# Performance work log

Measured on AMD Instinct MI355X. Metric: run time of the kernel, lower is better.

Reference implementation:

```python
import jax, jax.numpy as jnp
import numpy as np

GRID_SIZE = 5
SPLINE_ORDER = 3
GRID_RANGE = (-1.0, 1.0)
EPS = 1e-8


def _make_grid():
    h = (GRID_RANGE[1] - GRID_RANGE[0]) / GRID_SIZE
    # knots: [-spline_order, ..., grid_size + spline_order] * h + lo  -> 12 values
    return jnp.arange(-SPLINE_ORDER, GRID_SIZE + SPLINE_ORDER + 1, dtype=jnp.float32) * h + GRID_RANGE[0]


def _bspline_basis(x, grid):
    # x: [N, in]  ->  bases: [N, in, num_basis] with num_basis = grid_size + spline_order
    xe = x[..., None]                                   # [N, in, 1]
    bases = ((xe >= grid[:-1]) & (xe < grid[1:])).astype(x.dtype)  # [N, in, 11]
    for k in range(1, SPLINE_ORDER + 1):
        left = (xe - grid[: -(k + 1)]) / (grid[k:-1] - grid[: -(k + 1)] + EPS) * bases[..., :-1]
        right = (grid[k + 1:] - xe) / (grid[k + 1:] - grid[1:-k] + EPS) * bases[..., 1:]
        bases = left + right
    return bases                                        # [N, in, 8]


def setup_inputs() -> dict:
    key = jax.random.key(0)
    k1, k2, k3 = jax.random.split(key, 3)
    in_f, out_f, num_basis = 1024, 1024, GRID_SIZE + SPLINE_ORDER
    N = 4096
    x = jax.random.normal(k1, (N, in_f), dtype=jnp.float32)
    base_weight = jax.random.normal(k2, (out_f, in_f), dtype=jnp.float32) * (1.0 / np.sqrt(in_f))
    base_bias = jnp.zeros((out_f,), dtype=jnp.float32)
    spline_weight = jax.random.normal(k3, (out_f, in_f, num_basis), dtype=jnp.float32) * (1.0 / np.sqrt(in_f))
    return {"x": x, "base_weight": base_weight, "base_bias": base_bias, "spline_weight": spline_weight}


def reference(x, base_weight, base_bias, spline_weight):
    grid = _make_grid()
    # base path: SiLU(x) @ W_base^T + b
    base_out = jax.nn.silu(x) @ base_weight.T + base_bias          # [N, out]
    # spline path: Cox-de Boor basis then contraction over (in, basis)
    basis = _bspline_basis(x, grid)                                 # [N, in, 8]
    spline_out = jnp.einsum('nib,oib->no', basis, spline_weight)    # [N, out]
    return base_out + spline_out
```

## Files before the change

### kernel.cpp

```cpp
#include <hip/hip_runtime.h>
#include <hip/hip_bf16.h>
#include <stdint.h>

#define IN_F 1024
#define OUT_F 1024
#define NB 8
#define KDIM (IN_F + IN_F * NB)
#define NROWS 4096
#define SLICE_ELEMS (NROWS * OUT_F)
#define PREP_BLOCKS ((NROWS * IN_F) / 256)
#define WCONV_BLOCKS ((OUT_F * KDIM) / (4 * 256))

typedef __attribute__((ext_vector_type(8))) short bf16x8;
typedef __attribute__((ext_vector_type(4))) short bf16x4;
typedef __attribute__((ext_vector_type(4))) float f32x4;

__device__ __forceinline__ void bspline8(float x, float b8[8]) {
  float u = (x + 2.2f) * 2.5f;
  bool in = (u >= 0.0f) && (u < 11.0f);
  float uc = fminf(fmaxf(u, 0.0f), 10.99f);
  int i = (int)uc;
  float f = uc - (float)i;
  float g = 1.0f - f;
  float f2 = f * f, f3 = f2 * f;
  const float s = 1.0f / 6.0f;
  float v0 = f3 * s;
  float v1 = (-3.0f * f3 + 3.0f * f2 + 3.0f * f + 1.0f) * s;
  float v2 = (3.0f * f3 - 6.0f * f2 + 4.0f) * s;
  float v3 = g * g * g * s;
#pragma unroll
  for (int j = 0; j < 8; ++j) {
    int d = i - j;
    float r = (d == 0) ? v0 : (d == 1) ? v1 : (d == 2) ? v2 : (d == 3) ? v3 : 0.0f;
    b8[j] = in ? r : 0.0f;
  }
}

__global__ void prep_all_kernel(const float* __restrict__ x, const float* __restrict__ bw,
                                const float* __restrict__ sw, __hip_bfloat16* __restrict__ A,
                                __hip_bfloat16* __restrict__ W) {
  if (blockIdx.x < PREP_BLOCKS) {
    int idx = blockIdx.x * 256 + threadIdx.x;
    int n = idx >> 10;
    int i = idx & 1023;
    float xv = x[idx];
    float sl = xv / (1.0f + __expf(-xv));
    __hip_bfloat16* row = A + (size_t)n * KDIM;
    row[i] = __float2bfloat16(sl);
    float b8[8];
    bspline8(xv, b8);
    alignas(16) __hip_bfloat16 tmp[8];
#pragma unroll
    for (int c = 0; c < 8; ++c) tmp[c] = __float2bfloat16(b8[c]);
    *(bf16x8*)(row + IN_F + i * 8) = *(const bf16x8*)tmp;
  } else {
    int v = (blockIdx.x - PREP_BLOCKS) * 256 + threadIdx.x;
    int e = v * 4;
    int o = e / KDIM;
    int k = e - o * KDIM;
    float4 val = (k < IN_F) ? *(const float4*)(bw + o * IN_F + k)
                            : *(const float4*)(sw + (size_t)o * (IN_F * NB) + (k - IN_F));
    alignas(8) __hip_bfloat16 t[4];
    t[0] = __float2bfloat16(val.x);
    t[1] = __float2bfloat16(val.y);
    t[2] = __float2bfloat16(val.z);
    t[3] = __float2bfloat16(val.w);
    *(bf16x4*)(W + e) = *(const bf16x4*)t;
  }
}

__global__ __launch_bounds__(256) void gemm_kernel(const __hip_bfloat16* __restrict__ A,
                                                   const __hip_bfloat16* __restrict__ W,
                                                   float* __restrict__ dst,
                                                   const float* __restrict__ bias,
                                                   int kslice, int use_bias) {
  __shared__ __hip_bfloat16 lA[2][128 * 64];
  __shared__ __hip_bfloat16 lB[2][128 * 64];
  const int tid = threadIdx.x;
  const int wave = tid >> 6;
  const int lane = tid & 63;
  const int bm = blockIdx.x * 128;
  const int bn = blockIdx.y * 128;
  const int z = blockIdx.z;
  float* __restrict__ d = dst + (size_t)z * SLICE_ELEMS;
  const int kbeg = z * kslice;
  const int iters = kslice / 64;
  const int srow = lane & 15;
  const int skc = (lane >> 4) * 8;
  const int wm = (wave & 1) * 64;
  const int wn = (wave >> 1) * 64;
  const int r = lane & 15;
  const int quad = lane >> 4;

  const int g0 = wave * 2;
  const __hip_bfloat16* gA[2];
  const __hip_bfloat16* gB[2];
  gA[0] = A + (size_t)(bm + g0 * 16 + srow) * KDIM + kbeg + skc;
  gA[1] = gA[0] + (size_t)16 * KDIM;
  gB[0] = W + (size_t)(bn + g0 * 16 + srow) * KDIM + kbeg + skc;
  gB[1] = gB[0] + (size_t)16 * KDIM;

  f32x4 acc[4][4];
#pragma unroll
  for (int a = 0; a < 4; ++a)
#pragma unroll
    for (int b = 0; b < 4; ++b) acc[a][b] = (f32x4){0.f, 0.f, 0.f, 0.f};

#define STAGE(IT, BUF)                                                                             \
  do {                                                                                             \
    const int koff = (IT) * 64;                                                                    \
    _Pragma("unroll") for (int h = 0; h < 2; ++h) {                                                \
      _Pragma("unroll") for (int s = 0; s < 2; ++s) {                                              \
        const __hip_bfloat16* srcA = gA[h] + koff + s * 32;                                        \
        const __hip_bfloat16* srcB = gB[h] + koff + s * 32;                                        \
        __hip_bfloat16* dA = &lA[BUF][((g0 + h) * 2 + s) * 512];                                   \
        __hip_bfloat16* dB = &lB[BUF][((g0 + h) * 2 + s) * 512];                                   \
        __builtin_amdgcn_global_load_lds((const __attribute__((address_space(1))) void*)srcA,      \
                                         (__attribute__((address_space(3))) void*)dA, 16, 0, 0);   \
        __builtin_amdgcn_global_load_lds((const __attribute__((address_space(1))) void*)srcB,      \
                                         (__attribute__((address_space(3))) void*)dB, 16, 0, 0);   \
      }                                                                                            \
    }                                                                                              \
  } while (0)

  STAGE(0, 0);
  __syncthreads();

  for (int it = 0; it < iters; ++it) {
    const int p = it & 1;
    if (it + 1 < iters) STAGE(it + 1, p ^ 1);

#pragma unroll
    for (int s = 0; s < 2; ++s) {
      bf16x8 af[4], bfr[4];
#pragma unroll
      for (int t = 0; t < 4; ++t) {
        af[t] = *(const bf16x8*)&lA[p][(((wm >> 4) + t) * 2 + s) * 512 + lane * 8];
        bfr[t] = *(const bf16x8*)&lB[p][(((wn >> 4) + t) * 2 + s) * 512 + lane * 8];
      }
#pragma unroll
      for (int tm = 0; tm < 4; ++tm)
#pragma unroll
        for (int tn = 0; tn < 4; ++tn)
          acc[tm][tn] =
              __builtin_amdgcn_mfma_f32_16x16x32_bf16(af[tm], bfr[tn], acc[tm][tn], 0, 0, 0);
    }

    __syncthreads();
  }
#undef STAGE

#pragma unroll
  for (int tm = 0; tm < 4; ++tm) {
#pragma unroll
    for (int tn = 0; tn < 4; ++tn) {
      const int col = bn + wn + tn * 16 + r;
      const float bv = use_bias ? bias[col] : 0.0f;
#pragma unroll
      for (int reg = 0; reg < 4; ++reg) {
        const int rowi = bm + wm + tm * 16 + quad * 4 + reg;
        d[(size_t)rowi * OUT_F + col] = acc[tm][tn][reg] + bv;
      }
    }
  }
}

__global__ void reduce_kernel(const float* __restrict__ P, const float* __restrict__ bias,
                              float* __restrict__ out, int S) {
  int v = blockIdx.x * 256 + threadIdx.x;
  int e = v * 4;
  int o = e & (OUT_F - 1);
  float4 acc = *(const float4*)(bias + o);
  for (int s = 0; s < S; ++s) {
    float4 p = *(const float4*)(P + (size_t)s * SLICE_ELEMS + e);
    acc.x += p.x;
    acc.y += p.y;
    acc.z += p.z;
    acc.w += p.w;
  }
  *(float4*)(out + e) = acc;
}

__global__ void kan_fallback(const float* __restrict__ x, const float* __restrict__ bw,
                             const float* __restrict__ bb, const float* __restrict__ sw,
                             float* __restrict__ out) {
  __shared__ float act[KDIM];
  int n = blockIdx.x;
  for (int i = threadIdx.x; i < IN_F; i += 256) {
    float xv = x[(size_t)n * IN_F + i];
    act[i] = xv / (1.0f + __expf(-xv));
    float b8[8];
    bspline8(xv, b8);
#pragma unroll
    for (int c = 0; c < 8; ++c) act[IN_F + i * 8 + c] = b8[c];
  }
  __syncthreads();
  for (int o = threadIdx.x; o < OUT_F; o += 256) {
    float s = bb[o];
    const float* wbp = bw + (size_t)o * IN_F;
    for (int k = 0; k < IN_F; ++k) s += act[k] * wbp[k];
    const float* wsp = sw + (size_t)o * (IN_F * NB);
    for (int k = 0; k < IN_F * NB; ++k) s += act[IN_F + k] * wsp[k];
    out[(size_t)n * OUT_F + o] = s;
  }
}

extern "C" void kernel_launch(void* const* d_in, const int* in_sizes, int n_in, void* d_out,
                              int out_size, void* d_ws, size_t ws_size, hipStream_t stream) {
  const float* x = (const float*)d_in[0];
  const float* bw = (const float*)d_in[1];
  const float* bb = (const float*)d_in[2];
  const float* sw = (const float*)d_in[3];
  float* out = (float*)d_out;

  const size_t needA = (size_t)NROWS * KDIM * 2;
  const size_t needW = (size_t)OUT_F * KDIM * 2;
  const size_t sliceB = (size_t)SLICE_ELEMS * 4;
  if (ws_size < needA + needW) {
    kan_fallback<<<NROWS, 256, 0, stream>>>(x, bw, bb, sw, out);
    return;
  }
  __hip_bfloat16* A = (__hip_bfloat16*)d_ws;
  __hip_bfloat16* W = (__hip_bfloat16*)((char*)d_ws + needA);
  float* P = (float*)((char*)d_ws + needA + needW);
  const size_t avail = ws_size - needA - needW;
  int S = (avail >= 2 * sliceB) ? 2 : 1;

  prep_all_kernel<<<PREP_BLOCKS + WCONV_BLOCKS, 256, 0, stream>>>(x, bw, sw, A, W);
  if (S == 1) {
    gemm_kernel<<<dim3(NROWS / 128, OUT_F / 128, 1), 256, 0, stream>>>(A, W, out, bb, KDIM, 1);
  } else {
    gemm_kernel<<<dim3(NROWS / 128, OUT_F / 128, S), 256, 0, stream>>>(A, W, P, bb, KDIM / S, 0);
    reduce_kernel<<<SLICE_ELEMS / (4 * 256), 256, 0, stream>>>(P, bb, out, S);
  }
}
```

Before: 258.6 us.

## Use 256x256 tiles with split-K of four and atomic accumulation into output

The GEMM block tile grows from 128x128 to 256x256 with 512 threads, and each wave computes an 8x4 grid of 16x16 MFMA tiles. K is split four ways and partial results are added straight into the output with float atomics. The output is pre-initialised with the bias inside the prep kernel, so the partial-slice buffer and the separate reduce kernel go away. The larger tile raises arithmetic intensity per LDS byte but uses 128KB of LDS per block and more registers, which may limit occupancy. The atomics add contention and make the summation order non-deterministic.

```diff
diff --git a/kernel.cpp b/kernel.cpp
--- a/kernel.cpp
+++ b/kernel.cpp
@@ -8,8 +8,11 @@
 #define KDIM (IN_F + IN_F * NB)
 #define NROWS 4096
 #define SLICE_ELEMS (NROWS * OUT_F)
+#define INIT_BLOCKS (SLICE_ELEMS / (4 * 256))
 #define PREP_BLOCKS ((NROWS * IN_F) / 256)
 #define WCONV_BLOCKS ((OUT_F * KDIM) / (4 * 256))
+#define SPLIT 4
+#define KSLICE (KDIM / SPLIT)
 
 typedef __attribute__((ext_vector_type(8))) short bf16x8;
 typedef __attribute__((ext_vector_type(4))) short bf16x4;
@@ -37,10 +40,16 @@
 }
 
 __global__ void prep_all_kernel(const float* __restrict__ x, const float* __restrict__ bw,
-                                const float* __restrict__ sw, __hip_bfloat16* __restrict__ A,
-                                __hip_bfloat16* __restrict__ W) {
-  if (blockIdx.x < PREP_BLOCKS) {
-    int idx = blockIdx.x * 256 + threadIdx.x;
+                                const float* __restrict__ sw, const float* __restrict__ bb,
+                                __hip_bfloat16* __restrict__ A, __hip_bfloat16* __restrict__ W,
+                                float* __restrict__ out) {
+  if (blockIdx.x < INIT_BLOCKS) {
+    int v = blockIdx.x * 256 + threadIdx.x;
+    int e = v * 4;
+    int o = e & (OUT_F - 1);
+    *(float4*)(out + e) = *(const float4*)(bb + o);
+  } else if (blockIdx.x < INIT_BLOCKS + PREP_BLOCKS) {
+    int idx = (blockIdx.x - INIT_BLOCKS) * 256 + threadIdx.x;
     int n = idx >> 10;
     int i = idx & 1023;
     float xv = x[idx];
@@ -54,7 +63,7 @@
     for (int c = 0; c < 8; ++c) tmp[c] = __float2bfloat16(b8[c]);
     *(bf16x8*)(row + IN_F + i * 8) = *(const bf16x8*)tmp;
   } else {
-    int v = (blockIdx.x - PREP_BLOCKS) * 256 + threadIdx.x;
+    int v = (blockIdx.x - INIT_BLOCKS - PREP_BLOCKS) * 256 + threadIdx.x;
     int e = v * 4;
     int o = e / KDIM;
     int k = e - o * KDIM;
@@ -69,58 +78,53 @@
   }
 }
 
-__global__ __launch_bounds__(256) void gemm_kernel(const __hip_bfloat16* __restrict__ A,
-                                                   const __hip_bfloat16* __restrict__ W,
-                                                   float* __restrict__ dst,
-                                                   const float* __restrict__ bias,
-                                                   int kslice, int use_bias) {
-  __shared__ __hip_bfloat16 lA[2][128 * 64];
-  __shared__ __hip_bfloat16 lB[2][128 * 64];
+__global__ __launch_bounds__(512, 2) void gemm_kernel(const __hip_bfloat16* __restrict__ A,
+                                                      const __hip_bfloat16* __restrict__ W,
+                                                      float* __restrict__ out) {
+  __shared__ __hip_bfloat16 lA[2][256 * 64];
+  __shared__ __hip_bfloat16 lB[2][256 * 64];
   const int tid = threadIdx.x;
   const int wave = tid >> 6;
   const int lane = tid & 63;
-  const int bm = blockIdx.x * 128;
-  const int bn = blockIdx.y * 128;
-  const int z = blockIdx.z;
-  float* __restrict__ d = dst + (size_t)z * SLICE_ELEMS;
-  const int kbeg = z * kslice;
-  const int iters = kslice / 64;
+  const int bm = blockIdx.x * 256;
+  const int bn = blockIdx.y * 256;
+  const int kbeg = blockIdx.z * KSLICE;
+  const int iters = KSLICE / 64;
   const int srow = lane & 15;
   const int skc = (lane >> 4) * 8;
-  const int wm = (wave & 1) * 64;
-  const int wn = (wave >> 1) * 64;
+  const int wmi = wave & 1;
+  const int wni = wave >> 1;
   const int r = lane & 15;
   const int quad = lane >> 4;
 
-  const int g0 = wave * 2;
   const __hip_bfloat16* gA[2];
   const __hip_bfloat16* gB[2];
-  gA[0] = A + (size_t)(bm + g0 * 16 + srow) * KDIM + kbeg + skc;
+  gA[0] = A + (size_t)(bm + wave * 32 + srow) * KDIM + kbeg + skc;
   gA[1] = gA[0] + (size_t)16 * KDIM;
-  gB[0] = W + (size_t)(bn + g0 * 16 + srow) * KDIM + kbeg + skc;
+  gB[0] = W + (size_t)(bn + wave * 32 + srow) * KDIM + kbeg + skc;
   gB[1] = gB[0] + (size_t)16 * KDIM;
 
-  f32x4 acc[4][4];
-#pragma unroll
-  for (int a = 0; a < 4; ++a)
+  f32x4 acc[8][4];
+#pragma unroll
+  for (int a = 0; a < 8; ++a)
 #pragma unroll
     for (int b = 0; b < 4; ++b) acc[a][b] = (f32x4){0.f, 0.f, 0.f, 0.f};
 
-#define STAGE(IT, BUF)                                                                             \
-  do {                                                                                             \
-    const int koff = (IT) * 64;                                                                    \
-    _Pragma("unroll") for (int h = 0; h < 2; ++h) {                                                \
-      _Pragma("unroll") for (int s = 0; s < 2; ++s) {                                              \
-        const __hip_bfloat16* srcA = gA[h] + koff + s * 32;                                        \
-        const __hip_bfloat16* srcB = gB[h] + koff + s * 32;                                        \
-        __hip_bfloat16* dA = &lA[BUF][((g0 + h) * 2 + s) * 512];                                   \
-        __hip_bfloat16* dB = &lB[BUF][((g0 + h) * 2 + s) * 512];                                   \
-        __builtin_amdgcn_global_load_lds((const __attribute__((address_space(1))) void*)srcA,      \
-                                         (__attribute__((address_space(3))) void*)dA, 16, 0, 0);   \
-        __builtin_amdgcn_global_load_lds((const __attribute__((address_space(1))) void*)srcB,      \
-                                         (__attribute__((address_space(3))) void*)dB, 16, 0, 0);   \
-      }                                                                                            \
-    }                                                                                              \
+#define STAGE(IT, BUF)                                                                           \
+  do {                                                                                           \
+    const int koff = (IT) * 64;                                                                  \
+    _Pragma("unroll") for (int h = 0; h < 2; ++h) {                                              \
+      _Pragma("unroll") for (int s = 0; s < 2; ++s) {                                            \
+        const __hip_bfloat16* srcA = gA[h] + koff + s * 32;                                      \
+        const __hip_bfloat16* srcB = gB[h] + koff + s * 32;                                      \
+        __hip_bfloat16* dA = &lA[BUF][((wave * 2 + h) * 2 + s) * 512];                           \
+        __hip_bfloat16* dB = &lB[BUF][((wave * 2 + h) * 2 + s) * 512];                           \
+        __builtin_amdgcn_global_load_lds((const __attribute__((address_space(1))) void*)srcA,    \
+                                         (__attribute__((address_space(3))) void*)dA, 16, 0, 0); \
+        __builtin_amdgcn_global_load_lds((const __attribute__((address_space(1))) void*)srcB,    \
+                                         (__attribute__((address_space(3))) void*)dB, 16, 0, 0); \
+      }                                                                                          \
+    }                                                                                            \
   } while (0)
 
   STAGE(0, 0);
@@ -132,14 +136,15 @@
 
 #pragma unroll
     for (int s = 0; s < 2; ++s) {
-      bf16x8 af[4], bfr[4];
-#pragma unroll
-      for (int t = 0; t < 4; ++t) {
-        af[t] = *(const bf16x8*)&lA[p][(((wm >> 4) + t) * 2 + s) * 512 + lane * 8];
-        bfr[t] = *(const bf16x8*)&lB[p][(((wn >> 4) + t) * 2 + s) * 512 + lane * 8];
-      }
-#pragma unroll
-      for (int tm = 0; tm < 4; ++tm)
+      bf16x8 af[8], bfr[4];
+#pragma unroll
+      for (int t = 0; t < 8; ++t)
+        af[t] = *(const bf16x8*)&lA[p][(((wmi * 8 + t) * 2 + s)) * 512 + lane * 8];
+#pragma unroll
+      for (int t = 0; t < 4; ++t)
+        bfr[t] = *(const bf16x8*)&lB[p][(((wni * 4 + t) * 2 + s)) * 512 + lane * 8];
+#pragma unroll
+      for (int tm = 0; tm < 8; ++tm)
 #pragma unroll
         for (int tn = 0; tn < 4; ++tn)
           acc[tm][tn] =
@@ -151,34 +156,17 @@
 #undef STAGE
 
 #pragma unroll
-  for (int tm = 0; tm < 4; ++tm) {
+  for (int tm = 0; tm < 8; ++tm) {
 #pragma unroll
     for (int tn = 0; tn < 4; ++tn) {
-      const int col = bn + wn + tn * 16 + r;
-      const float bv = use_bias ? bias[col] : 0.0f;
+      const int col = bn + wni * 64 + tn * 16 + r;
 #pragma unroll
       for (int reg = 0; reg < 4; ++reg) {
-        const int rowi = bm + wm + tm * 16 + quad * 4 + reg;
-        d[(size_t)rowi * OUT_F + col] = acc[tm][tn][reg] + bv;
+        const int rowi = bm + wmi * 128 + tm * 16 + quad * 4 + reg;
+        atomicAdd(out + (size_t)rowi * OUT_F + col, acc[tm][tn][reg]);
       }
     }
   }
-}
-
-__global__ void reduce_kernel(const float* __restrict__ P, const float* __restrict__ bias,
-                              float* __restrict__ out, int S) {
-  int v = blockIdx.x * 256 + threadIdx.x;
-  int e = v * 4;
-  int o = e & (OUT_F - 1);
-  float4 acc = *(const float4*)(bias + o);
-  for (int s = 0; s < S; ++s) {
-    float4 p = *(const float4*)(P + (size_t)s * SLICE_ELEMS + e);
-    acc.x += p.x;
-    acc.y += p.y;
-    acc.z += p.z;
-    acc.w += p.w;
-  }
-  *(float4*)(out + e) = acc;
 }
 
 __global__ void kan_fallback(const float* __restrict__ x, const float* __restrict__ bw,
@@ -215,22 +203,14 @@
 
   const size_t needA = (size_t)NROWS * KDIM * 2;
   const size_t needW = (size_t)OUT_F * KDIM * 2;
-  const size_t sliceB = (size_t)SLICE_ELEMS * 4;
   if (ws_size < needA + needW) {
     kan_fallback<<<NROWS, 256, 0, stream>>>(x, bw, bb, sw, out);
     return;
   }
   __hip_bfloat16* A = (__hip_bfloat16*)d_ws;
   __hip_bfloat16* W = (__hip_bfloat16*)((char*)d_ws + needA);
-  float* P = (float*)((char*)d_ws + needA + needW);
-  const size_t avail = ws_size - needA - needW;
-  int S = (avail >= 2 * sliceB) ? 2 : 1;
-
-  prep_all_kernel<<<PREP_BLOCKS + WCONV_BLOCKS, 256, 0, stream>>>(x, bw, sw, A, W);
-  if (S == 1) {
-    gemm_kernel<<<dim3(NROWS / 128, OUT_F / 128, 1), 256, 0, stream>>>(A, W, out, bb, KDIM, 1);
-  } else {
-    gemm_kernel<<<dim3(NROWS / 128, OUT_F / 128, S), 256, 0, stream>>>(A, W, P, bb, KDIM / S, 0);
-    reduce_kernel<<<SLICE_ELEMS / (4 * 256), 256, 0, stream>>>(P, bb, out, S);
-  }
-}
+
+  prep_all_kernel<<<INIT_BLOCKS + PREP_BLOCKS + WCONV_BLOCKS, 256, 0, stream>>>(x, bw, sw, bb, A,
+                                                                                W, out);
+  gemm_kernel<<<dim3(NROWS / 256, OUT_F / 256, SPLIT), 512, 0, stream>>>(A, W, out);
+}
```

New measurement: 269.9 us. 4.4% more time.

## Replace LDS staging with direct register double-buffered global loads and split-K by three

Applied to the files above, without the earlier changes.

The GEMM no longer stages tiles through shared memory with async global-to-LDS loads. Each wave now loads its MFMA fragments directly from global memory into registers, with a two-step register double buffer, which removes barriers and LDS traffic. The K dimension is split three ways instead of two, and the iteration count becomes a template parameter. The cost is lost cross-wave reuse: each fragment is fetched from global/L2 by multiple waves, with short strided accesses.

```diff
diff --git a/kernel.cpp b/kernel.cpp
--- a/kernel.cpp
+++ b/kernel.cpp
@@ -69,36 +69,28 @@
   }
 }
 
+template <int ITERS>
 __global__ __launch_bounds__(256) void gemm_kernel(const __hip_bfloat16* __restrict__ A,
                                                    const __hip_bfloat16* __restrict__ W,
                                                    float* __restrict__ dst,
-                                                   const float* __restrict__ bias,
-                                                   int kslice, int use_bias) {
-  __shared__ __hip_bfloat16 lA[2][128 * 64];
-  __shared__ __hip_bfloat16 lB[2][128 * 64];
-  const int tid = threadIdx.x;
-  const int wave = tid >> 6;
-  const int lane = tid & 63;
+                                                   const float* __restrict__ bias, int use_bias) {
+  const int lane = threadIdx.x & 63;
+  const int wave = threadIdx.x >> 6;
   const int bm = blockIdx.x * 128;
   const int bn = blockIdx.y * 128;
-  const int z = blockIdx.z;
-  float* __restrict__ d = dst + (size_t)z * SLICE_ELEMS;
-  const int kbeg = z * kslice;
-  const int iters = kslice / 64;
-  const int srow = lane & 15;
-  const int skc = (lane >> 4) * 8;
+  const int kbeg = blockIdx.z * (ITERS * 32);
   const int wm = (wave & 1) * 64;
   const int wn = (wave >> 1) * 64;
   const int r = lane & 15;
   const int quad = lane >> 4;
 
-  const int g0 = wave * 2;
-  const __hip_bfloat16* gA[2];
-  const __hip_bfloat16* gB[2];
-  gA[0] = A + (size_t)(bm + g0 * 16 + srow) * KDIM + kbeg + skc;
-  gA[1] = gA[0] + (size_t)16 * KDIM;
-  gB[0] = W + (size_t)(bn + g0 * 16 + srow) * KDIM + kbeg + skc;
-  gB[1] = gB[0] + (size_t)16 * KDIM;
+  const __hip_bfloat16* pa[4];
+  const __hip_bfloat16* pb[4];
+#pragma unroll
+  for (int t = 0; t < 4; ++t) {
+    pa[t] = A + (size_t)(bm + wm + t * 16 + r) * KDIM + kbeg + quad * 8;
+    pb[t] = W + (size_t)(bn + wn + t * 16 + r) * KDIM + kbeg + quad * 8;
+  }
 
   f32x4 acc[4][4];
 #pragma unroll
@@ -106,50 +98,41 @@
 #pragma unroll
     for (int b = 0; b < 4; ++b) acc[a][b] = (f32x4){0.f, 0.f, 0.f, 0.f};
 
-#define STAGE(IT, BUF)                                                                             \
-  do {                                                                                             \
-    const int koff = (IT) * 64;                                                                    \
-    _Pragma("unroll") for (int h = 0; h < 2; ++h) {                                                \
-      _Pragma("unroll") for (int s = 0; s < 2; ++s) {                                              \
-        const __hip_bfloat16* srcA = gA[h] + koff + s * 32;                                        \
-        const __hip_bfloat16* srcB = gB[h] + koff + s * 32;                                        \
-        __hip_bfloat16* dA = &lA[BUF][((g0 + h) * 2 + s) * 512];                                   \
-        __hip_bfloat16* dB = &lB[BUF][((g0 + h) * 2 + s) * 512];                                   \
-        __builtin_amdgcn_global_load_lds((const __attribute__((address_space(1))) void*)srcA,      \
-                                         (__attribute__((address_space(3))) void*)dA, 16, 0, 0);   \
-        __builtin_amdgcn_global_load_lds((const __attribute__((address_space(1))) void*)srcB,      \
-                                         (__attribute__((address_space(3))) void*)dB, 16, 0, 0);   \
-      }                                                                                            \
-    }                                                                                              \
-  } while (0)
-
-  STAGE(0, 0);
-  __syncthreads();
-
-  for (int it = 0; it < iters; ++it) {
-    const int p = it & 1;
-    if (it + 1 < iters) STAGE(it + 1, p ^ 1);
-
-#pragma unroll
-    for (int s = 0; s < 2; ++s) {
-      bf16x8 af[4], bfr[4];
+  bf16x8 ca[4], cb[4], na[4], nb[4];
+#pragma unroll
+  for (int t = 0; t < 4; ++t) {
+    ca[t] = *(const bf16x8*)(pa[t]);
+    cb[t] = *(const bf16x8*)(pb[t]);
+  }
+
+  for (int it = 0; it < ITERS; it += 2) {
+#pragma unroll
+    for (int t = 0; t < 4; ++t) {
+      na[t] = *(const bf16x8*)(pa[t] + (it + 1) * 32);
+      nb[t] = *(const bf16x8*)(pb[t] + (it + 1) * 32);
+    }
+#pragma unroll
+    for (int tm = 0; tm < 4; ++tm)
+#pragma unroll
+      for (int tn = 0; tn < 4; ++tn)
+        acc[tm][tn] =
+            __builtin_amdgcn_mfma_f32_16x16x32_bf16(ca[tm], cb[tn], acc[tm][tn], 0, 0, 0);
+    if (it + 2 < ITERS) {
 #pragma unroll
       for (int t = 0; t < 4; ++t) {
-        af[t] = *(const bf16x8*)&lA[p][(((wm >> 4) + t) * 2 + s) * 512 + lane * 8];
-        bfr[t] = *(const bf16x8*)&lB[p][(((wn >> 4) + t) * 2 + s) * 512 + lane * 8];
+        ca[t] = *(const bf16x8*)(pa[t] + (it + 2) * 32);
+        cb[t] = *(const bf16x8*)(pb[t] + (it + 2) * 32);
       }
-#pragma unroll
-      for (int tm = 0; tm < 4; ++tm)
-#pragma unroll
-        for (int tn = 0; tn < 4; ++tn)
-          acc[tm][tn] =
-              __builtin_amdgcn_mfma_f32_16x16x32_bf16(af[tm], bfr[tn], acc[tm][tn], 0, 0, 0);
     }
-
-    __syncthreads();
-  }
-#undef STAGE
-
+#pragma unroll
+    for (int tm = 0; tm < 4; ++tm)
+#pragma unroll
+      for (int tn = 0; tn < 4; ++tn)
+        acc[tm][tn] =
+            __builtin_amdgcn_mfma_f32_16x16x32_bf16(na[tm], nb[tn], acc[tm][tn], 0, 0, 0);
+  }
+
+  float* __restrict__ d = dst + (size_t)blockIdx.z * SLICE_ELEMS;
 #pragma unroll
   for (int tm = 0; tm < 4; ++tm) {
 #pragma unroll
@@ -223,14 +206,13 @@
   __hip_bfloat16* A = (__hip_bfloat16*)d_ws;
   __hip_bfloat16* W = (__hip_bfloat16*)((char*)d_ws + needA);
   float* P = (float*)((char*)d_ws + needA + needW);
-  const size_t avail = ws_size - needA - needW;
-  int S = (avail >= 2 * sliceB) ? 2 : 1;
+  const bool split3 = (ws_size - needA - needW) >= 3 * sliceB;
 
   prep_all_kernel<<<PREP_BLOCKS + WCONV_BLOCKS, 256, 0, stream>>>(x, bw, sw, A, W);
-  if (S == 1) {
-    gemm_kernel<<<dim3(NROWS / 128, OUT_F / 128, 1), 256, 0, stream>>>(A, W, out, bb, KDIM, 1);
+  if (split3) {
+    gemm_kernel<96><<<dim3(NROWS / 128, OUT_F / 128, 3), 256, 0, stream>>>(A, W, P, bb, 0);
+    reduce_kernel<<<SLICE_ELEMS / (4 * 256), 256, 0, stream>>>(P, bb, out, 3);
   } else {
-    gemm_kernel<<<dim3(NROWS / 128, OUT_F / 128, S), 256, 0, stream>>>(A, W, P, bb, KDIM / S, 0);
-    reduce_kernel<<<SLICE_ELEMS / (4 * 256), 256, 0, stream>>>(P, bb, out, S);
-  }
-}
+    gemm_kernel<288><<<dim3(NROWS / 128, OUT_F / 128, 1), 256, 0, stream>>>(A, W, out, bb, 1);
+  }
+}
```

After: 384.7 us. 48.8% more time.
